# Performance work log

Measured on AMD Instinct MI355X. Metric: run time of the kernel, lower is better.

## Reference

```python
import jax, jax.numpy as jnp
import numpy as np

TOPK = 64  # topk_atoms
EPS = 1e-9


def setup_inputs() -> dict:
    key = jax.random.key(0)
    k1, k2 = jax.random.split(key)
    B, N = 32, 2048          # batch, num_atoms
    C, R = 64, 32            # channels, rank of low-rank factors U
    accumulated = jax.random.normal(k1, (B, N), dtype=jnp.float32)
    U = jax.random.normal(k2, (C, N, R), dtype=jnp.float32)
    return {"accumulated": accumulated, "U": U}


def reference(accumulated, U):
    # accumulated: [B, N]; U: [C, N, R]
    B, N = accumulated.shape
    C, _, R = U.shape
    K = min(TOPK, N)

    # ---- CoActivationComputer._compute: per-row top-k ----
    topk_vals, topk_idx = jax.lax.top_k(accumulated, K)  # [B,K], [B,K]

    # ---- CoActState.frob_inner_lowrank(U) ----
    U_t = jnp.transpose(U, (1, 2, 0))        # [N, R, C]
    U_topk = U_t[topk_idx]                   # [B, K, R, C] irregular gather
    Au = jnp.einsum('bk,bkrc->brc', topk_vals, U_topk)  # [B, R, C]
    frob = (Au ** 2).sum(axis=1) / (K * R + EPS)        # [B, C]

    # ---- CoActState.to_dense(): scatter_add of rank-1 outer products ----
    vals = topk_vals[:, :, None] * topk_vals[:, None, :]           # [B, K, K]
    flat_idx = (topk_idx[:, :, None] * N + topk_idx[:, None, :])   # [B, K, K]
    flat_idx = flat_idx.reshape(B, K * K)
    M = jnp.zeros((B, N * N), dtype=accumulated.dtype)
    M = M.at[jnp.arange(B)[:, None], flat_idx].add(vals.reshape(B, K * K))
    M = M.reshape(B, N, N)

    return topk_vals, topk_idx, frob, M
```

## Files before the change

kernel.cpp:

```cpp
#include <hip/hip_runtime.h>

#define B 32
#define N 2048
#define K 64
#define C 64
#define R 32

typedef float vf4 __attribute__((ext_vector_type(4)));

__device__ __forceinline__ unsigned long long kmax(unsigned long long a, unsigned long long b) {
    return a > b ? a : b;
}

#define ROWS_PER_BLOCK 8
#define ZERO_BLOCKS (B * (N / ROWS_PER_BLOCK))

__global__ __launch_bounds__(256) void fused_topk_zero_kernel(const float* __restrict__ acc,
                                                              float* __restrict__ out_vals,
                                                              float* __restrict__ out_idxf,
                                                              float* __restrict__ ws_vals,
                                                              int* __restrict__ ws_idx,
                                                              float* __restrict__ M) {
    const int t = threadIdx.x;

    if (blockIdx.x >= B) {
        const int zb = blockIdx.x - B;
        const int b = zb >> 8;
        const int rowblk = zb & 255;
        vf4* b4 = (vf4*)(M + ((size_t)b << 22) + ((size_t)rowblk << 14));
        const vf4 z = {0.f, 0.f, 0.f, 0.f};
#pragma unroll
        for (int j = 0; j < 16; ++j)
            __builtin_nontemporal_store(z, &b4[t + 256 * j]);
        return;
    }

    __shared__ unsigned long long wmax[4];
    const int b = blockIdx.x;
    const int lane = t & 63;
    const int wave = t >> 6;
    const float* row = acc + b * N;

    unsigned long long kr[8];
    unsigned long long m = 0ull;
#pragma unroll
    for (int j = 0; j < 8; ++j) {
        int i = t + 256 * j;
        unsigned int bits = __float_as_uint(row[i]);
        unsigned int u = (bits & 0x80000000u) ? ~bits : (bits | 0x80000000u);
        kr[j] = ((unsigned long long)u << 32) | (unsigned int)(N - 1 - i);
        m = kmax(m, kr[j]);
    }

    for (int s = 0; s < K; ++s) {
        unsigned long long w = m;
#pragma unroll
        for (int off = 32; off; off >>= 1)
            w = kmax(w, __shfl_down(w, off, 64));
        if (lane == 0) wmax[wave] = w;
        __syncthreads();
        unsigned long long best = kmax(kmax(wmax[0], wmax[1]), kmax(wmax[2], wmax[3]));
        if (t == 0) {
            unsigned int u = (unsigned int)(best >> 32);
            unsigned int bits = (u & 0x80000000u) ? (u ^ 0x80000000u) : ~u;
            float v = __uint_as_float(bits);
            int idx = (N - 1) - (int)(best & 0xFFFFFFFFull);
            out_vals[b * K + s] = v;
            out_idxf[b * K + s] = (float)idx;
            ws_vals[b * K + s] = v;
            ws_idx[b * K + s] = idx;
        }
        if (m == best) {
            unsigned long long nm = 0ull;
#pragma unroll
            for (int j = 0; j < 8; ++j) {
                if (kr[j] == best) kr[j] = 0ull;
                nm = kmax(nm, kr[j]);
            }
            m = nm;
        }
        __syncthreads();
    }
}

__global__ __launch_bounds__(256) void fused_frob_scatter_kernel(const float* __restrict__ U,
                                                                 const float* __restrict__ ws_vals,
                                                                 const int* __restrict__ ws_idx,
                                                                 float* __restrict__ out_frob,
                                                                 float* __restrict__ M) {
    const int t = threadIdx.x;

    if (blockIdx.x >= B * 8) {
        __shared__ float sv[K];
        __shared__ int si[K];
        const int b = blockIdx.x - B * 8;
        if (t < K) {
            sv[t] = ws_vals[b * K + t];
            si[t] = ws_idx[b * K + t];
        }
        __syncthreads();
        float* Mb = M + ((size_t)b << 22);
#pragma unroll
        for (int q = 0; q < 16; ++q) {
            int p = q * 256 + t;
            int i = p >> 6;
            int j = p & 63;
            Mb[(size_t)si[i] * N + si[j]] = sv[i] * sv[j];
        }
        return;
    }

    __shared__ float sv[K];
    __shared__ int si[K];
    const int b = blockIdx.x >> 3;
    const int cg = blockIdx.x & 7;
    if (t < K) {
        sv[t] = ws_vals[b * K + t];
        si[t] = ws_idx[b * K + t];
    }
    __syncthreads();
    const int r = t & 31;
    const int c = (cg << 3) + (t >> 5);
    const float* Uc = U + (size_t)c * (N * R) + r;
    float accv = 0.0f;
#pragma unroll 8
    for (int k = 0; k < K; ++k)
        accv = fmaf(sv[k], Uc[(size_t)si[k] * R], accv);
    float x = accv * accv;
#pragma unroll
    for (int off = 16; off; off >>= 1)
        x += __shfl_xor(x, off, 32);
    if (r == 0) out_frob[b * C + c] = x * (1.0f / 2048.0f);
}

extern "C" void kernel_launch(void* const* d_in, const int* in_sizes, int n_in,
                              void* d_out, int out_size, void* d_ws, size_t ws_size,
                              hipStream_t stream) {
    const float* acc = (const float*)d_in[0];
    const float* U = (const float*)d_in[1];
    float* out = (float*)d_out;

    float* out_vals = out;
    float* out_idxf = out + B * K;
    float* out_frob = out + 2 * B * K;
    float* out_M = out + 3 * B * K;

    float* ws_vals = (float*)d_ws;
    int* ws_idx = (int*)((char*)d_ws + B * K * sizeof(float));

    fused_topk_zero_kernel<<<B + ZERO_BLOCKS, 256, 0, stream>>>(acc, out_vals, out_idxf,
                                                                ws_vals, ws_idx, out_M);
    fused_frob_scatter_kernel<<<B * 8 + B, 256, 0, stream>>>(U, ws_vals, ws_idx,
                                                             out_frob, out_M);
}
```

Before: 563.1 us.

## Move M zeroing into frob kernel and fuse per-row scatter into zero blocks

Splits top-k into its own kernel and moves the zeroing of the dense M matrix into the second kernel. Each zero block loads the top-k indices, finds which of its 8 rows are selected, zeroes the rows, then writes the outer-product entries for those rows after a barrier. This removes the separate scatter blocks and the write-after-zero ordering across kernels. In exchange, zeroing no longer overlaps with the serial top-k kernel, which now runs alone on 32 blocks.

```diff
diff --git a/kernel.cpp b/kernel.cpp
--- a/kernel.cpp
+++ b/kernel.cpp
@@ -12,30 +12,13 @@
     return a > b ? a : b;
 }
 
-#define ROWS_PER_BLOCK 8
-#define ZERO_BLOCKS (B * (N / ROWS_PER_BLOCK))
-
-__global__ __launch_bounds__(256) void fused_topk_zero_kernel(const float* __restrict__ acc,
-                                                              float* __restrict__ out_vals,
-                                                              float* __restrict__ out_idxf,
-                                                              float* __restrict__ ws_vals,
-                                                              int* __restrict__ ws_idx,
-                                                              float* __restrict__ M) {
+__global__ __launch_bounds__(256) void topk_kernel(const float* __restrict__ acc,
+                                                   float* __restrict__ out_vals,
+                                                   float* __restrict__ out_idxf,
+                                                   float* __restrict__ ws_vals,
+                                                   int* __restrict__ ws_idx) {
+    __shared__ unsigned long long wmax[4];
     const int t = threadIdx.x;
-
-    if (blockIdx.x >= B) {
-        const int zb = blockIdx.x - B;
-        const int b = zb >> 8;
-        const int rowblk = zb & 255;
-        vf4* b4 = (vf4*)(M + ((size_t)b << 22) + ((size_t)rowblk << 14));
-        const vf4 z = {0.f, 0.f, 0.f, 0.f};
-#pragma unroll
-        for (int j = 0; j < 16; ++j)
-            __builtin_nontemporal_store(z, &b4[t + 256 * j]);
-        return;
-    }
-
-    __shared__ unsigned long long wmax[4];
     const int b = blockIdx.x;
     const int lane = t & 63;
     const int wave = t >> 6;
@@ -83,35 +66,54 @@
     }
 }
 
-__global__ __launch_bounds__(256) void fused_frob_scatter_kernel(const float* __restrict__ U,
-                                                                 const float* __restrict__ ws_vals,
-                                                                 const int* __restrict__ ws_idx,
-                                                                 float* __restrict__ out_frob,
-                                                                 float* __restrict__ M) {
+#define FROB_BLOCKS (B * 8)
+#define ZERO_BLOCKS (B * (N / 8))
+
+__global__ __launch_bounds__(256) void fused_frob_zero_insert_kernel(const float* __restrict__ U,
+                                                                     const float* __restrict__ ws_vals,
+                                                                     const int* __restrict__ ws_idx,
+                                                                     float* __restrict__ out_frob,
+                                                                     float* __restrict__ M) {
+    __shared__ float sv[K];
+    __shared__ int si[K];
     const int t = threadIdx.x;
 
-    if (blockIdx.x >= B * 8) {
-        __shared__ float sv[K];
-        __shared__ int si[K];
-        const int b = blockIdx.x - B * 8;
+    if (blockIdx.x >= FROB_BLOCKS) {
+        __shared__ int match[8];
+        const int zb = blockIdx.x - FROB_BLOCKS;
+        const int b = zb >> 8;
+        const int rowblk = zb & 255;
+        const int row0 = rowblk * 8;
+
         if (t < K) {
             sv[t] = ws_vals[b * K + t];
             si[t] = ws_idx[b * K + t];
         }
+        if (t < 8) match[t] = -1;
         __syncthreads();
-        float* Mb = M + ((size_t)b << 22);
+        if (t < K) {
+            int d = si[t] - row0;
+            if (d >= 0 && d < 8) match[d] = t;
+        }
+
+        float* base = M + ((size_t)b << 22) + ((size_t)row0 << 11);
+        vf4* b4 = (vf4*)base;
+        const vf4 z = {0.f, 0.f, 0.f, 0.f};
 #pragma unroll
-        for (int q = 0; q < 16; ++q) {
-            int p = q * 256 + t;
-            int i = p >> 6;
-            int j = p & 63;
-            Mb[(size_t)si[i] * N + si[j]] = sv[i] * sv[j];
+        for (int j = 0; j < 16; ++j)
+            __builtin_nontemporal_store(z, &b4[t + 256 * j]);
+
+        __syncthreads();
+
+#pragma unroll
+        for (int rr = 0; rr < 8; ++rr) {
+            int p = match[rr];
+            if (p >= 0 && t < K)
+                base[(size_t)rr * N + si[t]] = sv[p] * sv[t];
         }
         return;
     }
 
-    __shared__ float sv[K];
-    __shared__ int si[K];
     const int b = blockIdx.x >> 3;
     const int cg = blockIdx.x & 7;
     if (t < K) {
@@ -148,8 +150,7 @@
     float* ws_vals = (float*)d_ws;
     int* ws_idx = (int*)((char*)d_ws + B * K * sizeof(float));
 
-    fused_topk_zero_kernel<<<B + ZERO_BLOCKS, 256, 0, stream>>>(acc, out_vals, out_idxf,
-                                                                ws_vals, ws_idx, out_M);
-    fused_frob_scatter_kernel<<<B * 8 + B, 256, 0, stream>>>(U, ws_vals, ws_idx,
-                                                             out_frob, out_M);
+    topk_kernel<<<B, 256, 0, stream>>>(acc, out_vals, out_idxf, ws_vals, ws_idx);
+    fused_frob_zero_insert_kernel<<<FROB_BLOCKS + ZERO_BLOCKS, 256, 0, stream>>>(
+        U, ws_vals, ws_idx, out_frob, out_M);
 }
```

Result: slower. 596.3 us (+5.9%).
